# Optimization experiments

Hardware: AMD Instinct MI355X
Metric: run time of the kernel (lower is better)

Reference implementation:

```python
import jax, jax.numpy as jnp
import numpy as np

D_MODEL = 192; D_INNER = 384; N_STATE = 16; D_CONV = 4; DT_RANK = 12; DEPTH = 24
PATCH = 16; STRIDE = 16; IMG = 128; EPS = 1e-5


def _ln(x, w, b):
    m = jnp.mean(x, -1, keepdims=True)
    v = jnp.mean((x - m) ** 2, -1, keepdims=True)
    return (x - m) * jax.lax.rsqrt(v + EPS) * w + b


def _mamba_dir(xz, cw, cb, xpw, dpw, dpb, Alog, Dv):
    # xz: (B, L, 2*d_inner); one direction of the bidirectional Mamba mixer
    xp, z = jnp.split(xz, 2, axis=-1)               # (B,L,di) each
    xc = jnp.transpose(xp, (0, 2, 1))               # (B,di,L)
    xc = jnp.pad(xc, ((0, 0), (0, 0), (D_CONV - 1, 0)))  # causal pad
    xc = jax.lax.conv_general_dilated(
        xc, cw, (1,), 'VALID',
        dimension_numbers=('NCH', 'OIH', 'NCH'),
        feature_group_count=D_INNER) + cb[None, :, None]
    u = jax.nn.silu(jnp.transpose(xc, (0, 2, 1)))   # (B,L,di)
    dbl = u @ xpw.T                                  # (B,L,dt_rank+2N)
    dt, Bm, Cm = jnp.split(dbl, [DT_RANK, DT_RANK + N_STATE], axis=-1)
    dt = jax.nn.softplus(dt @ dpw.T + dpb)           # (B,L,di)
    A = -jnp.exp(Alog)                               # (di,N)
    dA = jnp.exp(dt[..., None] * A)                  # (B,L,di,N)
    dBu = (dt * u)[..., None] * Bm[:, :, None, :]    # (B,L,di,N)

    def comb(c1, c2):
        a1, b1 = c1
        a2, b2 = c2
        return a1 * a2, a2 * b1 + b2

    _, h = jax.lax.associative_scan(comb, (dA, dBu), axis=1)
    y = jnp.einsum('bldn,bln->bld', h, Cm) + u * Dv
    return y * jax.nn.silu(z)


def _forward(x, patch_w, patch_b, ln_w, ln_b, in_w,
             cf_w, cf_b, xpf_w, dtf_w, dtf_b, Alog_f, D_f,
             cbk_w, cbk_b, xpb_w, dtb_w, dtb_b, Alog_b, D_b,
             out_w, nf_w, nf_b, head_w, head_b):
    B = x.shape[0]
    p = jax.lax.conv_general_dilated(
        x, patch_w, (STRIDE,) * 3, 'VALID',
        dimension_numbers=('NCDHW', 'OIDHW', 'NCDHW')) + patch_b[None, :, None, None, None]
    hidden = p.reshape(B, D_MODEL, -1).transpose(0, 2, 1)  # (B, L=512, D)
    residual = jnp.zeros_like(hidden)

    xs = (ln_w, ln_b, in_w, cf_w, cf_b, xpf_w, dtf_w, dtf_b, Alog_f, D_f,
          cbk_w, cbk_b, xpb_w, dtb_w, dtb_b, Alog_b, D_b, out_w)

    def step(carry, pl):
        hidden, residual = carry
        (lw, lb, iw, cfw, cfb, xpf, dwf, dbf, Af, Dfv,
         cbw, cbb, xpb, dwb, dbb, Ab, Dbv, ow) = pl
        residual = residual + hidden
        hn = _ln(residual, lw, lb)
        xz = hn @ iw.T                               # (B,L,2di)
        yf = _mamba_dir(xz, cfw, cfb, xpf, dwf, dbf, Af, Dfv)
        yb = jnp.flip(_mamba_dir(jnp.flip(xz, 1), cbw, cbb, xpb, dwb, dbb, Ab, Dbv), 1)
        hidden = (yf + yb) @ ow.T
        return (hidden, residual), None

    (hidden, residual), _ = jax.lax.scan(step, (hidden, residual), xs)
    final = _ln(residual + hidden, nf_w, nf_b)
    feat = final[:, -1, :]                           # final_pool_type='none' -> last token
    return feat @ head_w.T + head_b


def setup_inputs() -> dict:
    key = jax.random.key(0)
    ks = jax.random.split(key, 16)
    rn = lambda k, s, sc=0.02: jax.random.normal(k, s, jnp.float32) * sc
    d = {}
    d['x'] = jax.random.normal(ks[0], (1, 1, IMG, IMG, IMG), jnp.float32)
    d['patch_w'] = rn(ks[1], (D_MODEL, 1, PATCH, PATCH, PATCH), 0.05)
    d['patch_b'] = jnp.zeros((D_MODEL,), jnp.float32)
    d['ln_w'] = jnp.ones((DEPTH, D_MODEL), jnp.float32)
    d['ln_b'] = jnp.zeros((DEPTH, D_MODEL), jnp.float32)
    d['in_w'] = rn(ks[2], (DEPTH, 2 * D_INNER, D_MODEL))
    d['cf_w'] = rn(ks[3], (DEPTH, D_INNER, 1, D_CONV), 0.2)
    d['cf_b'] = jnp.zeros((DEPTH, D_INNER), jnp.float32)
    d['xpf_w'] = rn(ks[4], (DEPTH, DT_RANK + 2 * N_STATE, D_INNER))
    d['dtf_w'] = rn(ks[5], (DEPTH, D_INNER, DT_RANK), 0.1)
    d['dtf_b'] = jnp.full((DEPTH, D_INNER), -4.6, jnp.float32)  # softplus -> dt~0.01
    d['Alog_f'] = jnp.log(jnp.broadcast_to(jnp.arange(1, N_STATE + 1, dtype=jnp.float32), (DEPTH, D_INNER, N_STATE)))
    d['D_f'] = jnp.ones((DEPTH, D_INNER), jnp.float32)
    d['cbk_w'] = rn(ks[6], (DEPTH, D_INNER, 1, D_CONV), 0.2)
    d['cbk_b'] = jnp.zeros((DEPTH, D_INNER), jnp.float32)
    d['xpb_w'] = rn(ks[7], (DEPTH, DT_RANK + 2 * N_STATE, D_INNER))
    d['dtb_w'] = rn(ks[8], (DEPTH, D_INNER, DT_RANK), 0.1)
    d['dtb_b'] = jnp.full((DEPTH, D_INNER), -4.6, jnp.float32)
    d['Alog_b'] = jnp.log(jnp.broadcast_to(jnp.arange(1, N_STATE + 1, dtype=jnp.float32), (DEPTH, D_INNER, N_STATE)))
    d['D_b'] = jnp.ones((DEPTH, D_INNER), jnp.float32)
    d['out_w'] = rn(ks[9], (DEPTH, D_MODEL, D_INNER))
    d['nf_w'] = jnp.ones((D_MODEL,), jnp.float32)
    d['nf_b'] = jnp.zeros((D_MODEL,), jnp.float32)
    d['head_w'] = rn(ks[10], (2, D_MODEL))
    d['head_b'] = jnp.zeros((2,), jnp.float32)
    return d


def reference(x, patch_w, patch_b, ln_w, ln_b, in_w,
              cf_w, cf_b, xpf_w, dtf_w, dtf_b, Alog_f, D_f,
              cbk_w, cbk_b, xpb_w, dtb_w, dtb_b, Alog_b, D_b,
              out_w, nf_w, nf_b, head_w, head_b):
    return _forward(x, patch_w, patch_b, ln_w, ln_b, in_w,
                    cf_w, cf_b, xpf_w, dtf_w, dtf_b, Alog_f, D_f,
                    cbk_w, cbk_b, xpb_w, dtb_w, dtb_b, Alog_b, D_b,
                    out_w, nf_w, nf_b, head_w, head_b)
```

## Files before the change

### kernel.cpp

```cpp
#include <hip/hip_runtime.h>
#include <hip/hip_bf16.h>

#define D_MODEL 192
#define D_INNER 384
#define N_STATE 16
#define DT_RANK 12
#define DEPTH 24
#define SEQ 512
#define NCHUNK 8
#define CLEN 64
#define TS 68
#define AS 33
#define PART_STRIDE (SEQ * D_MODEL)
#define USTR (SEQ * D_INNER)
#define KSPLIT 16
#define NBLK 512
#define FSTR 32

typedef __hip_bfloat16 bf16;
typedef unsigned short u16;
typedef unsigned long long u64;

__device__ __forceinline__ float silu_f(float x) { return x / (1.f + __expf(-x)); }
__device__ __forceinline__ float softplus_f(float x) {
    return (x > 20.f) ? x : log1pf(__expf(x));
}
__device__ __forceinline__ float bf2f(unsigned u) {
    return __uint_as_float(u << 16);
}
__device__ __forceinline__ u16 f2bu(float f) {
    bf16 b = __float2bfloat16(f);
    return *reinterpret_cast<u16*>(&b);
}

__device__ __forceinline__ float aload(const float* p) {
    return __hip_atomic_load(p, __ATOMIC_RELAXED, __HIP_MEMORY_SCOPE_AGENT);
}
__device__ __forceinline__ void astore(float* p, float v) {
    __hip_atomic_store(p, v, __ATOMIC_RELAXED, __HIP_MEMORY_SCOPE_AGENT);
}
__device__ __forceinline__ unsigned aloadu(const unsigned* p) {
    return __hip_atomic_load(p, __ATOMIC_RELAXED, __HIP_MEMORY_SCOPE_AGENT);
}
__device__ __forceinline__ void astoreu(unsigned* p, unsigned v) {
    __hip_atomic_store(p, v, __ATOMIC_RELAXED, __HIP_MEMORY_SCOPE_AGENT);
}
__device__ __forceinline__ float2 aload2(const float* p) {
    const u64 v = __hip_atomic_load((const u64*)p, __ATOMIC_RELAXED, __HIP_MEMORY_SCOPE_AGENT);
    return make_float2(__uint_as_float((unsigned)v), __uint_as_float((unsigned)(v >> 32)));
}
__device__ __forceinline__ void astore2(float* p, float x, float y) {
    const u64 v = (u64)__float_as_uint(x) | ((u64)__float_as_uint(y) << 32);
    __hip_atomic_store((u64*)p, v, __ATOMIC_RELAXED, __HIP_MEMORY_SCOPE_AGENT);
}
__device__ __forceinline__ float4 aload4v(const float* p) {
    const float2 a = aload2(p), b = aload2(p + 2);
    return make_float4(a.x, a.y, b.x, b.y);
}
__device__ __forceinline__ void astore4v(float* p, float4 v) {
    astore2(p, v.x, v.y); astore2(p + 2, v.z, v.w);
}

template<typename T> __device__ __forceinline__ float ld(const void* p, long i) {
    return ((const float*)p)[i];
}
template<> __device__ __forceinline__ float ld<bf16>(const void* p, long i) {
    return bf2f(((const u16*)p)[i]);
}
template<typename T> __device__ __forceinline__ float4 ld4(const void* p, long i) {
    return *(const float4*)((const float*)p + i);
}
template<> __device__ __forceinline__ float4 ld4<bf16>(const void* p, long i) {
    const ushort4 v = *(const ushort4*)((const u16*)p + i);
    return make_float4(bf2f(v.x), bf2f(v.y), bf2f(v.z), bf2f(v.w));
}
template<typename T> __device__ __forceinline__ void st(void* p, int i, float v) {
    ((float*)p)[i] = v;
}
template<> __device__ __forceinline__ void st<bf16>(void* p, int i, float v) {
    ((bf16*)p)[i] = __float2bfloat16(v);
}
__device__ __forceinline__ float dot4(const float4& a, const float4& b) {
    return a.x * b.x + a.y * b.y + a.z * b.z + a.w * b.w;
}
__device__ __forceinline__ void ld8b(const u16* p, float4& a, float4& b) {
    const uint4 u = *(const uint4*)p;
    a.x = bf2f(u.x & 0xffffu); a.y = bf2f(u.x >> 16);
    a.z = bf2f(u.y & 0xffffu); a.w = bf2f(u.y >> 16);
    b.x = bf2f(u.z & 0xffffu); b.y = bf2f(u.z >> 16);
    b.z = bf2f(u.w & 0xffffu); b.w = bf2f(u.w >> 16);
}
__device__ __forceinline__ float4 ld4b(const u16* p) {
    const uint2 u = *(const uint2*)p;
    return make_float4(bf2f(u.x & 0xffffu), bf2f(u.x >> 16),
                       bf2f(u.y & 0xffffu), bf2f(u.y >> 16));
}

__device__ __forceinline__ void post_flag(unsigned* fl, unsigned v, int tid) {
    asm volatile("s_waitcnt vmcnt(0)" ::: "memory");
    __syncthreads();
    if (tid == 0) astoreu(fl, v);
}
__device__ __forceinline__ void wait_flag(const unsigned* fl, unsigned v) {
    int spins = 0;
    while (aloadu(fl) < v) {
        if (++spins > (1 << 20)) break;
        __builtin_amdgcn_s_sleep(1);
    }
}

__device__ __forceinline__ void gbar(unsigned* bar, unsigned target, bool fence) {
    asm volatile("s_waitcnt vmcnt(0)" ::: "memory");
    __syncthreads();
    const int bid = blockIdx.x, tid = threadIdx.x;
    unsigned* gen0 = bar + 512 * FSTR;
    if (tid == 0) {
        if (fence) __threadfence();
        astoreu(&bar[bid * FSTR], target);
    }
    if (bid == 0) {
        int spins = 0;
        for (;;) {
            const unsigned va = aloadu(&bar[tid * FSTR]);
            const unsigned vb = aloadu(&bar[(tid + 256) * FSTR]);
            const bool ok = (va >= target) && (vb >= target);
            if (__syncthreads_and(ok)) break;
            if (++spins > (1 << 20)) break;
            __builtin_amdgcn_s_sleep(1);
        }
        if (tid == 0) astoreu(gen0, target);
    } else if (tid == 0) {
        int spins = 0;
        if (bid < 16) {
            while (aloadu(gen0) < target) {
                if (++spins > (1 << 20)) break;
                __builtin_amdgcn_s_sleep(2);
            }
            astoreu(&gen0[bid * FSTR], target);
        } else if (bid < 32) {
            while (aloadu(gen0) < target) {
                if (++spins > (1 << 20)) break;
                __builtin_amdgcn_s_sleep(2);
            }
        } else {
            unsigned* rl = &gen0[(bid >> 5) * FSTR];
            while (aloadu(rl) < target) {
                if (++spins > (1 << 20)) break;
                __builtin_amdgcn_s_sleep(2);
            }
        }
    }
    if (fence && tid == 0) __threadfence();
    __syncthreads();
}

__device__ void cvtB(const void* s, u16* d, long n, long g, long str, int isb) {
    if (isb) {
        const u16* p = (const u16*)s;
        for (long i = g * 4; i < n; i += str * 4) *(ushort4*)(d + i) = *(const ushort4*)(p + i);
    } else {
        const float* p = (const float*)s;
        for (long i = g * 4; i < n; i += str * 4) {
            const float4 v = *(const float4*)(p + i);
            ushort4 o; o.x = f2bu(v.x); o.y = f2bu(v.y); o.z = f2bu(v.z); o.w = f2bu(v.w);
            *(ushort4*)(d + i) = o;
        }
    }
}
__device__ void cvtF(const void* s, float* d, long n, long g, long str, int isb) {
    if (isb) {
        const u16* p = (const u16*)s;
        for (long i = g * 4; i < n; i += str * 4) {
            const ushort4 v = *(const ushort4*)(p + i);
            *(float4*)(d + i) = make_float4(bf2f(v.x), bf2f(v.y), bf2f(v.z), bf2f(v.w));
        }
    } else {
        const float* p = (const float*)s;
        for (long i = g * 4; i < n; i += str * 4) *(float4*)(d + i) = *(const float4*)(p + i);
    }
}
__device__ void cvtNA(const void* s, float* d, long n, long g, long str, int isb) {
    if (isb) {
        const u16* p = (const u16*)s;
        for (long i = g * 4; i < n; i += str * 4) {
            const ushort4 v = *(const ushort4*)(p + i);
            *(float4*)(d + i) = make_float4(-__expf(bf2f(v.x)), -__expf(bf2f(v.y)),
                                            -__expf(bf2f(v.z)), -__expf(bf2f(v.w)));
        }
    } else {
        const float* p = (const float*)s;
        for (long i = g * 4; i < n; i += str * 4) {
            const float4 v = *(const float4*)(p + i);
            *(float4*)(d + i) = make_float4(-__expf(v.x), -__expf(v.y), -__expf(v.z), -__expf(v.w));
        }
    }
}

template<typename T>
__device__ void final_phase(int tid, const float* res, const float* y, const void* ow,
                            const void* nw, const void* nb, const void* hw, const void* hb,
                            void* out, float* syf, float* f, float* red) {
    for (int i = tid; i < D_INNER; i += 256)
        syf[i] = aload(&y[(long)511 * D_INNER + i]) + aload(&y[(long)USTR + 511 * D_INNER + i]);
    __syncthreads();
    float v = 0.f;
    if (tid < D_MODEL) {
        float acc = 0.f;
        const long wrow = (long)(DEPTH - 1) * D_MODEL * D_INNER + (long)tid * D_INNER;
        for (int k = 0; k < D_INNER; k += 4)
            acc += dot4(ld4<T>(ow, wrow + k), *(const float4*)&syf[k]);
        v = aload(&res[511 * D_MODEL + tid]) + acc;
    }
    float s = v;
    #pragma unroll
    for (int o = 32; o > 0; o >>= 1) s += __shfl_down(s, o, 64);
    if ((tid & 63) == 0 && tid < D_MODEL) red[tid >> 6] = s;
    __syncthreads();
    const float mean = (red[0] + red[1] + red[2]) * (1.f / D_MODEL);
    const float d = (tid < D_MODEL) ? (v - mean) : 0.f;
    float s2 = d * d;
    #pragma unroll
    for (int o = 32; o > 0; o >>= 1) s2 += __shfl_down(s2, o, 64);
    if ((tid & 63) == 0 && tid < D_MODEL) red[3 + (tid >> 6)] = s2;
    __syncthreads();
    const float var = (red[3] + red[4] + red[5]) * (1.f / D_MODEL);
    if (tid < D_MODEL)
        f[tid] = d * rsqrtf(var + 1e-5f) * ld<T>(nw, tid) + ld<T>(nb, tid);
    __syncthreads();
    if (tid < 2) {
        float a2 = ld<T>(hb, tid);
        for (int c = 0; c < D_MODEL; ++c) a2 += f[c] * ld<T>(hw, tid * D_MODEL + c);
        st<T>(out, tid, a2);
    }
}

struct MegaArgs {
    const void *x, *pw, *pb, *lnw, *lnb, *inw, *cfw, *cfb, *xpfw, *dtfw, *dtfb, *Af, *Dfv;
    const void *cbw, *cbb, *xpbw, *dtbw, *dtbb, *Ab, *Dbv, *ow, *nfw, *nfb, *hw, *hb;
    void* out;
    unsigned* bar;
    float *hidC, *res0, *res1, *xz, *u, *dbl, *dt, *y, *chunkH, *chunkP;
    float *lnwF, *lnbF, *cbfF, *cbbF, *dtbfF, *dtbbF, *negAfF, *negAbF, *DfF, *DbF, *pbF;
    u16 *inwB, *owB, *xB, *pwB, *xpwfB, *xpwbB, *dtwfB, *dtwbB, *cwfB, *cwbB;
};

__global__ void init_kernel(unsigned* bar) {
    const int i = blockIdx.x * 256 + threadIdx.x;
    ((uint4*)bar)[i] = make_uint4(0, 0, 0, 0);
}

__global__ void __launch_bounds__(256, 2) mega_kernel(MegaArgs a) {
    __shared__ float smem[6144];
    const int bid = blockIdx.x;
    const int tid = threadIdx.x;
    unsigned* bar = a.bar;
    unsigned* scanR = a.bar + 528 * FSTR;
    unsigned* aflag = a.bar + 912 * FSTR;
    unsigned* bflag = a.bar + 1168 * FSTR;
    unsigned gen_ctr = 0;
    const int isb = (((const unsigned*)a.lnw)[0] != 0x3F800000u);

    {
        const long g = (long)bid * 256 + tid;
        const long str = (long)NBLK * 256;
        cvtB(a.inw,  a.inwB,  3538944, g, str, isb);
        cvtB(a.ow,   a.owB,   1769472, g, str, isb);
        cvtB(a.x,    a.xB,    2097152, g, str, isb);
        cvtB(a.pw,   a.pwB,    786432, g, str, isb);
        cvtB(a.xpfw, a.xpwfB,  405504, g, str, isb);
        cvtB(a.xpbw, a.xpwbB,  405504, g, str, isb);
        cvtB(a.dtfw, a.dtwfB,  110592, g, str, isb);
        cvtB(a.dtbw, a.dtwbB,  110592, g, str, isb);
        cvtB(a.cfw,  a.cwfB,    36864, g, str, isb);
        cvtB(a.cbw,  a.cwbB,    36864, g, str, isb);
        cvtF(a.lnw,  a.lnwF,     4608, g, str, isb);
        cvtF(a.lnb,  a.lnbF,     4608, g, str, isb);
        cvtF(a.cfb,  a.cbfF,     9216, g, str, isb);
        cvtF(a.cbb,  a.cbbF,     9216, g, str, isb);
        cvtF(a.dtfb, a.dtbfF,    9216, g, str, isb);
        cvtF(a.dtbb, a.dtbbF,    9216, g, str, isb);
        cvtF(a.pb,   a.pbF,       192, g, str, isb);
        cvtNA(a.Af,  a.negAfF,  147456, g, str, isb);
        cvtNA(a.Ab,  a.negAbF,  147456, g, str, isb);
        cvtF(a.Dfv,  a.DfF,      9216, g, str, isb);
        cvtF(a.Dbv,  a.DbF,      9216, g, str, isb);
    }
    gbar(bar, ++gen_ctr, true);

    {
        float* As_ = smem;
        float* Ws  = smem + 1056;
        const int ty = tid >> 4, tx = tid & 15;
        for (int unit = bid; unit < 768; unit += NBLK) {
            const int mt = unit & 15, nt = (unit >> 4) % 3, ks = unit / 48;
            const int m0 = mt * 32, n0 = nt * 64, kk0 = ks * 256;
            float acc[2][4] = {};
            for (int kk = kk0; kk < kk0 + 256; kk += 32) {
                for (int e = tid; e < 1024; e += 256) {
                    const int m = e >> 5, k = e & 31;
                    const int kid = kk + k, t = m0 + m;
                    const int dz = kid >> 8, dy = (kid >> 4) & 15, dx = kid & 15;
                    const int pz = t >> 6, py = (t >> 3) & 7, px = t & 7;
                    As_[k * AS + m] = bf2f(a.xB[(long)(pz * 16 + dz) * 16384 + (py * 16 + dy) * 128 + (px * 16 + dx)]);
                }
                for (int e = tid; e < 2048; e += 256) {
                    const int n = e >> 5, k = e & 31;
                    Ws[k * TS + n] = bf2f(a.pwB[(long)(n0 + n) * 4096 + kk + k]);
                }
                __syncthreads();
                #pragma unroll 8
                for (int k = 0; k < 32; ++k) {
                    const float a0 = As_[k * AS + ty * 2];
                    const float a1 = As_[k * AS + ty * 2 + 1];
                    const float4 w4 = *(const float4*)&Ws[k * TS + tx * 4];
                    acc[0][0] += a0 * w4.x; acc[0][1] += a0 * w4.y;
                    acc[0][2] += a0 * w4.z; acc[0][3] += a0 * w4.w;
                    acc[1][0] += a1 * w4.x; acc[1][1] += a1 * w4.y;
                    acc[1][2] += a1 * w4.z; acc[1][3] += a1 * w4.w;
                }
                __syncthreads();
            }
            float* C = a.hidC + (long)ks * PART_STRIDE;
            #pragma unroll
            for (int i = 0; i < 2; ++i) {
                float4 o4 = make_float4(acc[i][0], acc[i][1], acc[i][2], acc[i][3]);
                if (ks == 0) {
                    o4.x += a.pbF[n0 + tx * 4 + 0];
                    o4.y += a.pbF[n0 + tx * 4 + 1];
                    o4.z += a.pbF[n0 + tx * 4 + 2];
                    o4.w += a.pbF[n0 + tx * 4 + 3];
                }
                astore4v(&C[(m0 + ty * 2 + i) * D_MODEL + n0 + tx * 4], o4);
            }
        }
    }
    gbar(bar, ++gen_ctr, false);

    const int ch = tid >> 4, np = tid & 15;
    float* sU  = smem;
    float* sDT = smem + 1024;
    float* sBC = smem + 2048;
    float* sZ  = smem + 4096;
    float* sY  = smem + 5120;

    for (int l = 0; l < DEPTH; ++l) {
        const int first = (l == 0);
        const unsigned lv = (unsigned)(l + 1);
        const float* resIn = (l & 1) ? a.res1 : a.res0;
        float* resOut      = (l & 1) ? a.res0 : a.res1;

        if (bid < 256) {
            float* sy  = smem;
            float* lnS = smem + 768;
            float* hnS = smem + 1152;
            const int t0 = bid * 2;
            if (!first) {
                for (int j = tid; j < 384; j += 256) {
                    const int tt = j / 192, d2 = (j - tt * 192) * 2;
                    const long o = (long)(t0 + tt) * D_INNER + d2;
                    const float2 v1 = aload2(&a.y[o]);
                    const float2 v2 = aload2(&a.y[(long)USTR + o]);
                    sy[tt * D_INNER + d2]     = v1.x + v2.x;
                    sy[tt * D_INNER + d2 + 1] = v1.y + v2.y;
                }
            }
            __syncthreads();
            if (tid < D_MODEL) {
                float accB[2];
                if (first) {
                    #pragma unroll
                    for (int tt = 0; tt < 2; ++tt) {
                        float s = 0.f;
                        #pragma unroll
                        for (int sp = 0; sp < KSPLIT; ++sp)
                            s += aload(&a.hidC[(long)sp * PART_STRIDE + (t0 + tt) * D_MODEL + tid]);
                        accB[tt] = s;
                    }
                } else {
                    accB[0] = accB[1] = 0.f;
                    const u16* wr = a.owB + (long)(l - 1) * D_MODEL * D_INNER + (long)tid * D_INNER;
                    for (int k = 0; k < D_INNER; k += 8) {
                        float4 va, vb;
                        ld8b(wr + k, va, vb);
                        accB[0] += dot4(va, *(const float4*)&sy[k]) + dot4(vb, *(const float4*)&sy[k + 4]);
                        accB[1] += dot4(va, *(const float4*)&sy[D_INNER + k]) + dot4(vb, *(const float4*)&sy[D_INNER + k + 4]);
                    }
                }
                #pragma unroll
                for (int tt = 0; tt < 2; ++tt) {
                    const float rv = accB[tt] + (first ? 0.f : aload(&resIn[(t0 + tt) * D_MODEL + tid]));
                    lnS[tt * D_MODEL + tid] = rv;
                    astore(&resOut[(t0 + tt) * D_MODEL + tid], rv);
                }
            }
            __syncthreads();
            {
                const int w = tid >> 6, lane = tid & 63;
                if (w < 2) {
                    const float v0 = lnS[w * D_MODEL + lane];
                    const float v1 = lnS[w * D_MODEL + lane + 64];
                    const float v2 = lnS[w * D_MODEL + lane + 128];
                    float s = v0 + v1 + v2;
                    #pragma unroll
                    for (int o = 32; o > 0; o >>= 1) s += __shfl_xor(s, o, 64);
                    const float mean = s * (1.f / D_MODEL);
                    const float d0 = v0 - mean, d1 = v1 - mean, d2 = v2 - mean;
                    float s2 = d0 * d0 + d1 * d1 + d2 * d2;
                    #pragma unroll
                    for (int o = 32; o > 0; o >>= 1) s2 += __shfl_xor(s2, o, 64);
                    const float rstd = rsqrtf(s2 * (1.f / D_MODEL) + 1e-5f);
                    hnS[w * D_MODEL + lane]       = d0 * rstd * a.lnwF[l * D_MODEL + lane]       + a.lnbF[l * D_MODEL + lane];
                    hnS[w * D_MODEL + lane + 64]  = d1 * rstd * a.lnwF[l * D_MODEL + lane + 64]  + a.lnbF[l * D_MODEL + lane + 64];
                    hnS[w * D_MODEL + lane + 128] = d2 * rstd * a.lnwF[l * D_MODEL + lane + 128] + a.lnbF[l * D_MODEL + lane + 128];
                }
            }
            __syncthreads();
            float accD[3][2] = {};
            const u16* w0 = a.inwB + (long)l * 2 * D_INNER * D_MODEL;
            for (int k = 0; k < D_MODEL; k += 8) {
                #pragma unroll
                for (int r = 0; r < 3; ++r) {
                    float4 va, vb;
                    ld8b(w0 + (long)(tid + r * 256) * D_MODEL + k, va, vb);
                    #pragma unroll
                    for (int tt = 0; tt < 2; ++tt) {
                        accD[r][tt] += dot4(va, *(const float4*)&hnS[tt * D_MODEL + k])
                                     + dot4(vb, *(const float4*)&hnS[tt * D_MODEL + k + 4]);
                    }
                }
            }
            #pragma unroll
            for (int r = 0; r < 3; ++r)
                #pragma unroll
                for (int tt = 0; tt < 2; ++tt)
                    astore(&a.xz[(long)(t0 + tt) * 2 * D_INNER + tid + r * 256], accD[r][tt]);
            post_flag(&aflag[bid * FSTR], lv, tid);
        }

        {
            const int dir = bid >> 8, bb = bid & 255;
            int lo, hi;
            if (dir == 0) { lo = bb >= 2 ? bb - 2 : 0; hi = bb; }
            else { lo = bb <= 255 ? (255 - bb > 0 ? 255 - bb : 0) : 0;
                   hi = 257 - bb <= 255 ? 257 - bb : 255; }
            if (tid <= hi - lo) wait_flag(&aflag[(lo + tid) * FSTR], lv);
            __syncthreads();

            float* su   = smem;
            float* dblP = smem + 768;
            float* dblS = smem + 960;
            const u16* cwB   = dir ? a.cwbB  : a.cwfB;
            const float* cbF = dir ? a.cbbF  : a.cbfF;
            const u16* xpwB  = dir ? a.xpwbB : a.xpwfB;
            const u16* dtwB  = dir ? a.dtwbB : a.dtwfB;
            const float* dtbF = dir ? a.dtbbF : a.dtbfF;
            const int t0 = bb * 2;
            float* ub = a.u + (long)dir * USTR;
            for (int j = tid; j < 384; j += 256) {
                const int tt = j / 192, d2 = (j - tt * 192) * 2;
                const int t = t0 + tt;
                float4 wa, wb;
                ld8b(cwB + (long)(l * D_INNER + d2) * 4, wa, wb);
                const float cw0[4] = {wa.x, wa.y, wa.z, wa.w};
                const float cw1[4] = {wb.x, wb.y, wb.z, wb.w};
                float acc0 = cbF[l * D_INNER + d2];
                float acc1 = cbF[l * D_INNER + d2 + 1];
                #pragma unroll
                for (int k = 0; k < 4; ++k) {
                    const int ii = t + k - 3;
                    if (ii >= 0) {
                        const int src = dir ? (511 - ii) : ii;
                        const float2 xv = aload2(&a.xz[(long)src * 2 * D_INNER + d2]);
                        acc0 += xv.x * cw0[k];
                        acc1 += xv.y * cw1[k];
                    }
                }
                const float u0 = silu_f(acc0), u1 = silu_f(acc1);
                su[tt * D_INNER + d2] = u0;
                su[tt * D_INNER + d2 + 1] = u1;
                astore2(&ub[(long)t * D_INNER + d2], u0, u1);
            }
            __syncthreads();
            if (tid < 176) {
                const int half = tid / 88;
                const int r = tid - half * 88;
                const int tt = r / 44, out = r - tt * 44;
                const u16* wr = xpwB + (long)(l * 44 + out) * D_INNER;
                const int k0 = half * 192;
                float acc = 0.f;
                for (int k = k0; k < k0 + 192; k += 8) {
                    float4 va, vb;
                    ld8b(wr + k, va, vb);
                    acc += dot4(va, *(const float4*)&su[tt * D_INNER + k])
                         + dot4(vb, *(const float4*)&su[tt * D_INNER + k + 4]);
                }
                dblP[half * 96 + tt * 48 + out] = acc;
            }
            __syncthreads();
            if (tid < 88) {
                const int tt = tid / 44, out = tid - tt * 44;
                const float s = dblP[tt * 48 + out] + dblP[96 + tt * 48 + out];
                dblS[tt * 48 + out] = s;
                astore(&a.dbl[(long)dir * SEQ * 44 + (long)(t0 + tt) * 44 + out], s);
            }
            __syncthreads();
            float* dtp = a.dt + (long)dir * USTR;
            for (int j = tid; j < 384; j += 256) {
                const int tt = j / 192, d2 = (j - tt * 192) * 2;
                const u16* wr = dtwB + (long)(l * D_INNER + d2) * DT_RANK;
                float4 A0, B0; ld8b(wr, A0, B0);
                const float4 C0 = ld4b(wr + 8);
                float4 A1, B1; ld8b(wr + 12, A1, B1);
                const float4 C1 = ld4b(wr + 20);
                const float* ds = &dblS[tt * 48];
                const float4 ds0 = *(const float4*)ds;
                const float4 ds1 = *(const float4*)(ds + 4);
                const float4 ds2 = *(const float4*)(ds + 8);
                const float acc0 = dtbF[l * D_INNER + d2]
                    + dot4(A0, ds0) + dot4(B0, ds1) + dot4(C0, ds2);
                const float acc1 = dtbF[l * D_INNER + d2 + 1]
                    + dot4(A1, ds0) + dot4(B1, ds1) + dot4(C1, ds2);
                astore2(&dtp[(long)(t0 + tt) * D_INNER + d2],
                        softplus_f(acc0), softplus_f(acc1));
            }
            post_flag(&bflag[bid * FSTR], lv, tid);
        }

        if (bid < 384) {
            const int dg = bid % 24, chunk = (bid / 24) & 7, dir2 = bid / 192;
            if (tid < 32) wait_flag(&bflag[(dir2 * 256 + chunk * 32 + tid) * FSTR], lv);
            __syncthreads();
            const int d0 = dg * 16, d = d0 + ch;
            const int t0s = chunk * CLEN;
            const float* ub  = a.u  + (long)dir2 * USTR;
            const float* dtp = a.dt + (long)dir2 * USTR;
            const float* db  = a.dbl + (long)dir2 * SEQ * 44;
            {
                const int t = tid >> 2, dl4 = (tid & 3) * 4;
                const int tg = t0s + t;
                const long base = (long)tg * D_INNER + d0 + dl4;
                *(float4*)&sU[t * 16 + dl4]  = aload4v(&ub[base]);
                *(float4*)&sDT[t * 16 + dl4] = aload4v(&dtp[base]);
                const int out_l = dir2 ? (511 - tg) : tg;
                *(float4*)&sZ[t * 16 + dl4] = aload4v(&a.xz[(long)out_l * 2 * D_INNER + D_INNER + d0 + dl4]);
            }
            for (int i = tid; i < 512; i += 256) {
                const int t = i >> 3, j4 = (i & 7) * 4;
                *(float4*)&sBC[t * 32 + j4] = aload4v(&db[(long)(t0s + t) * 44 + DT_RANK + j4]);
            }
            const float* negA = dir2 ? a.negAbF : a.negAfF;
            const float Areg = negA[(long)(l * D_INNER + d) * N_STATE + np];
            const float Dval = (dir2 ? a.DbF : a.DfF)[l * D_INNER + d];
            __syncthreads();
            float h = 0.f, dts = 0.f;
            for (int t = 0; t < CLEN; ++t) {
                const float dtv = sDT[t * 16 + ch];
                h = __expf(dtv * Areg) * h + (dtv * sU[t * 16 + ch]) * sBC[t * 32 + np];
                dts += dtv;
            }
            const long cb = ((long)(dir2 * NCHUNK + chunk) * D_INNER + d) * N_STATE + np;
            astore(&a.chunkH[cb], h);
            astore(&a.chunkP[cb], __expf(Areg * dts));
            post_flag(&scanR[((dir2 * NCHUNK + chunk) * 24 + dg) * FSTR], lv, tid);
            if (tid < chunk) wait_flag(&scanR[((dir2 * NCHUNK + tid) * 24 + dg) * FSTR], lv);
            __syncthreads();
            float hs[NCHUNK - 1], ps[NCHUNK - 1];
            #pragma unroll
            for (int c = 0; c < NCHUNK - 1; ++c) {
                if (c < chunk) {
                    const long cbb = ((long)(dir2 * NCHUNK + c) * D_INNER + d) * N_STATE + np;
                    hs[c] = aload(&a.chunkH[cbb]);
                    ps[c] = aload(&a.chunkP[cbb]);
                }
            }
            float h0 = 0.f;
            #pragma unroll
            for (int c = 0; c < NCHUNK - 1; ++c)
                if (c < chunk) h0 = ps[c] * h0 + hs[c];
            h = h0;
            for (int t = 0; t < CLEN; ++t) {
                const float dtv = sDT[t * 16 + ch];
                const float uv = sU[t * 16 + ch];
                h = __expf(dtv * Areg) * h + (dtv * uv) * sBC[t * 32 + np];
                float part = h * sBC[t * 32 + 16 + np];
                part += __shfl_xor(part, 1, 64);
                part += __shfl_xor(part, 2, 64);
                part += __shfl_xor(part, 4, 64);
                part += __shfl_xor(part, 8, 64);
                if (np == 0)
                    sY[t * 16 + ch] = (part + uv * Dval) * silu_f(sZ[t * 16 + ch]);
            }
            __syncthreads();
            {
                const int t = tid >> 2, dl4 = (tid & 3) * 4;
                const int tg = t0s + t;
                const int out_l = dir2 ? (511 - tg) : tg;
                float* yb = a.y + (long)dir2 * USTR;
                astore4v(&yb[(long)out_l * D_INNER + d0 + dl4], *(float4*)&sY[t * 16 + dl4]);
            }
        }
        gbar(bar, ++gen_ctr, false);
    }

    if (bid == 0) {
        float* syf = smem;
        float* f   = smem + 384;
        float* red = smem + 576;
        if (isb) final_phase<bf16>(tid, a.res0, a.y, a.ow, a.nfw, a.nfb, a.hw, a.hb, a.out, syf, f, red);
        else     final_phase<float>(tid, a.res0, a.y, a.ow, a.nfw, a.nfb, a.hw, a.hb, a.out, syf, f, red);
    }
}

extern "C" void kernel_launch(void* const* d_in, const int* in_sizes, int n_in,
                              void* d_out, int out_size, void* d_ws, size_t ws_size,
                              hipStream_t stream) {
    (void)in_sizes; (void)n_in; (void)out_size; (void)ws_size;
    const void* x    = d_in[0];
    const void* pw   = d_in[1];
    const void* pb   = d_in[2];
    const void* lnw  = d_in[3];
    const void* lnb  = d_in[4];
    const void* inw  = d_in[5];
    const void* cfw  = d_in[6];
    const void* cfb  = d_in[7];
    const void* xpfw = d_in[8];
    const void* dtfw = d_in[9];
    const void* dtfb = d_in[10];
    const void* Af   = d_in[11];
    const void* Dfv  = d_in[12];
    const void* cbw  = d_in[13];
    const void* cbb  = d_in[14];
    const void* xpbw = d_in[15];
    const void* dtbw = d_in[16];
    const void* dtbb = d_in[17];
    const void* Ab   = d_in[18];
    const void* Dbv  = d_in[19];
    const void* ow   = d_in[20];
    const void* nfw  = d_in[21];
    const void* nfb  = d_in[22];
    const void* hw   = d_in[23];
    const void* hb   = d_in[24];

    unsigned* bar = (unsigned*)d_ws;
    float* w = (float*)((char*)d_ws + 262144);
    float* hidC   = w;  w += KSPLIT * PART_STRIDE;
    float* res0   = w;  w += PART_STRIDE;
    float* res1   = w;  w += PART_STRIDE;
    float* xz     = w;  w += SEQ * 2 * D_INNER;
    float* u      = w;  w += 2 * USTR;
    float* dbl    = w;  w += 2 * SEQ * 44;
    float* dt     = w;  w += 2 * USTR;
    float* y      = w;  w += 2 * USTR;
    float* chunkH = w;  w += 2 * NCHUNK * D_INNER * N_STATE;
    float* chunkP = w;  w += 2 * NCHUNK * D_INNER * N_STATE;
    float* lnwF = w;  w += 4608;
    float* lnbF = w;  w += 4608;
    float* cbfF = w;  w += 9216;
    float* cbbF = w;  w += 9216;
    float* dtbfF = w; w += 9216;
    float* dtbbF = w; w += 9216;
    float* negAfF = w; w += 147456;
    float* negAbF = w; w += 147456;
    float* DfF = w;   w += 9216;
    float* DbF = w;   w += 9216;
    float* pbF = w;   w += 192;
    u16* b = (u16*)w;
    u16* inwB  = b;  b += 3538944;
    u16* owB   = b;  b += 1769472;
    u16* xB    = b;  b += 2097152;
    u16* pwB   = b;  b += 786432;
    u16* xpwfB = b;  b += 405504;
    u16* xpwbB = b;  b += 405504;
    u16* dtwfB = b;  b += 110592;
    u16* dtwbB = b;  b += 110592;
    u16* cwfB  = b;  b += 36864;
    u16* cwbB  = b;  b += 36864;

    MegaArgs ma;
    ma.x = x; ma.pw = pw; ma.pb = pb; ma.lnw = lnw; ma.lnb = lnb; ma.inw = inw;
    ma.cfw = cfw; ma.cfb = cfb; ma.xpfw = xpfw; ma.dtfw = dtfw; ma.dtfb = dtfb;
    ma.Af = Af; ma.Dfv = Dfv; ma.cbw = cbw; ma.cbb = cbb; ma.xpbw = xpbw;
    ma.dtbw = dtbw; ma.dtbb = dtbb; ma.Ab = Ab; ma.Dbv = Dbv; ma.ow = ow;
    ma.nfw = nfw; ma.nfb = nfb; ma.hw = hw; ma.hb = hb; ma.out = d_out;
    ma.bar = bar;
    ma.hidC = hidC; ma.res0 = res0; ma.res1 = res1; ma.xz = xz; ma.u = u;
    ma.dbl = dbl; ma.dt = dt; ma.y = y; ma.chunkH = chunkH; ma.chunkP = chunkP;
    ma.lnwF = lnwF; ma.lnbF = lnbF; ma.cbfF = cbfF; ma.cbbF = cbbF;
    ma.dtbfF = dtbfF; ma.dtbbF = dtbbF; ma.negAfF = negAfF; ma.negAbF = negAbF;
    ma.DfF = DfF; ma.DbF = DbF; ma.pbF = pbF;
    ma.inwB = inwB; ma.owB = owB; ma.xB = xB; ma.pwB = pwB;
    ma.xpwfB = xpwfB; ma.xpwbB = xpwbB; ma.dtwfB = dtwfB; ma.dtwbB = dtwbB;
    ma.cwfB = cwfB; ma.cwbB = cwbB;

    init_kernel<<<64, 256, 0, stream>>>(bar);
    mega_kernel<<<NBLK, 256, 0, stream>>>(ma);
}
```

Baseline: 1.955 ms.

## Replace every other per-layer grid barrier with fine-grained y flags and double buffers

Per-chunk y-ready flags are added so that the next layer's LN/in-proj blocks wait only for the scan chunks they consume, instead of a global grid barrier after every layer. The barrier now runs only on odd layers. Intermediate buffers (xz, u, dt, dbl, chunk states) are double-buffered by layer parity so adjacent layers cannot overwrite each other's data. This costs extra workspace and flag traffic, and risks races if the parity and flag dependencies are incomplete.

```diff
diff --git a/kernel.cpp b/kernel.cpp
--- a/kernel.cpp
+++ b/kernel.cpp
@@ -16,6 +16,8 @@
 #define KSPLIT 16
 #define NBLK 512
 #define FSTR 32
+#define XZSTR (SEQ * 2 * D_INNER)
+#define CHSTR (2 * NCHUNK * D_INNER * N_STATE)
 
 typedef __hip_bfloat16 bf16;
 typedef unsigned short u16;
@@ -257,6 +259,7 @@
     unsigned* scanR = a.bar + 528 * FSTR;
     unsigned* aflag = a.bar + 912 * FSTR;
     unsigned* bflag = a.bar + 1168 * FSTR;
+    unsigned* yflag = a.bar + 1680 * FSTR;
     unsigned gen_ctr = 0;
     const int isb = (((const unsigned*)a.lnw)[0] != 0x3F800000u);
 
@@ -346,10 +349,27 @@
     for (int l = 0; l < DEPTH; ++l) {
         const int first = (l == 0);
         const unsigned lv = (unsigned)(l + 1);
-        const float* resIn = (l & 1) ? a.res1 : a.res0;
-        float* resOut      = (l & 1) ? a.res0 : a.res1;
+        const int par = l & 1;
+        float* xzP = a.xz + (long)par * XZSTR;
+        float* uP  = a.u  + (long)par * (2 * USTR);
+        float* dtP = a.dt + (long)par * (2 * USTR);
+        float* dbG = a.dbl + (long)par * (2 * SEQ * 44);
+        float* chH = a.chunkH + (long)par * CHSTR;
+        float* chPb = a.chunkP + (long)par * CHSTR;
+        const float* resIn = par ? a.res1 : a.res0;
+        float* resOut      = par ? a.res0 : a.res1;
 
         if (bid < 256) {
+            if (par) {
+                if (tid < 48) {
+                    const int dd = tid / 24, dg = tid - dd * 24;
+                    const int cf = bid >> 5;
+                    const int cb = (511 - 2 * bid) >> 6;
+                    const int cc = dd ? cb : cf;
+                    wait_flag(&yflag[((dd * NCHUNK + cc) * 24 + dg) * FSTR], (unsigned)l);
+                }
+                __syncthreads();
+            }
             float* sy  = smem;
             float* lnS = smem + 768;
             float* hnS = smem + 1152;
@@ -433,7 +453,7 @@
             for (int r = 0; r < 3; ++r)
                 #pragma unroll
                 for (int tt = 0; tt < 2; ++tt)
-                    astore(&a.xz[(long)(t0 + tt) * 2 * D_INNER + tid + r * 256], accD[r][tt]);
+                    astore(&xzP[(long)(t0 + tt) * 2 * D_INNER + tid + r * 256], accD[r][tt]);
             post_flag(&aflag[bid * FSTR], lv, tid);
         }
 
@@ -455,7 +475,7 @@
             const u16* dtwB  = dir ? a.dtwbB : a.dtwfB;
             const float* dtbF = dir ? a.dtbbF : a.dtbfF;
             const int t0 = bb * 2;
-            float* ub = a.u + (long)dir * USTR;
+            float* ub = uP + (long)dir * USTR;
             for (int j = tid; j < 384; j += 256) {
                 const int tt = j / 192, d2 = (j - tt * 192) * 2;
                 const int t = t0 + tt;
@@ -470,7 +490,7 @@
                     const int ii = t + k - 3;
                     if (ii >= 0) {
                         const int src = dir ? (511 - ii) : ii;
-                        const float2 xv = aload2(&a.xz[(long)src * 2 * D_INNER + d2]);
+                        const float2 xv = aload2(&xzP[(long)src * 2 * D_INNER + d2]);
                         acc0 += xv.x * cw0[k];
                         acc1 += xv.y * cw1[k];
                     }
@@ -501,10 +521,10 @@
                 const int tt = tid / 44, out = tid - tt * 44;
                 const float s = dblP[tt * 48 + out] + dblP[96 + tt * 48 + out];
                 dblS[tt * 48 + out] = s;
-                astore(&a.dbl[(long)dir * SEQ * 44 + (long)(t0 + tt) * 44 + out], s);
-            }
-            __syncthreads();
-            float* dtp = a.dt + (long)dir * USTR;
+                astore(&dbG[(long)dir * SEQ * 44 + (long)(t0 + tt) * 44 + out], s);
+            }
+            __syncthreads();
+            float* dtp = dtP + (long)dir * USTR;
             for (int j = tid; j < 384; j += 256) {
                 const int tt = j / 192, d2 = (j - tt * 192) * 2;
                 const u16* wr = dtwB + (long)(l * D_INNER + d2) * DT_RANK;
@@ -532,9 +552,9 @@
             __syncthreads();
             const int d0 = dg * 16, d = d0 + ch;
             const int t0s = chunk * CLEN;
-            const float* ub  = a.u  + (long)dir2 * USTR;
-            const float* dtp = a.dt + (long)dir2 * USTR;
-            const float* db  = a.dbl + (long)dir2 * SEQ * 44;
+            const float* ub  = uP  + (long)dir2 * USTR;
+            const float* dtp = dtP + (long)dir2 * USTR;
+            const float* db  = dbG + (long)dir2 * SEQ * 44;
             {
                 const int t = tid >> 2, dl4 = (tid & 3) * 4;
                 const int tg = t0s + t;
@@ -542,7 +562,7 @@
                 *(float4*)&sU[t * 16 + dl4]  = aload4v(&ub[base]);
                 *(float4*)&sDT[t * 16 + dl4] = aload4v(&dtp[base]);
                 const int out_l = dir2 ? (511 - tg) : tg;
-                *(float4*)&sZ[t * 16 + dl4] = aload4v(&a.xz[(long)out_l * 2 * D_INNER + D_INNER + d0 + dl4]);
+                *(float4*)&sZ[t * 16 + dl4] = aload4v(&xzP[(long)out_l * 2 * D_INNER + D_INNER + d0 + dl4]);
             }
             for (int i = tid; i < 512; i += 256) {
                 const int t = i >> 3, j4 = (i & 7) * 4;
@@ -558,9 +578,9 @@
                 h = __expf(dtv * Areg) * h + (dtv * sU[t * 16 + ch]) * sBC[t * 32 + np];
                 dts += dtv;
             }
-            const long cb = ((long)(dir2 * NCHUNK + chunk) * D_INNER + d) * N_STATE + np;
-            astore(&a.chunkH[cb], h);
-            astore(&a.chunkP[cb], __expf(Areg * dts));
+            const long cb2 = ((long)(dir2 * NCHUNK + chunk) * D_INNER + d) * N_STATE + np;
+            astore(&chH[cb2], h);
+            astore(&chPb[cb2], __expf(Areg * dts));
             post_flag(&scanR[((dir2 * NCHUNK + chunk) * 24 + dg) * FSTR], lv, tid);
             if (tid < chunk) wait_flag(&scanR[((dir2 * NCHUNK + tid) * 24 + dg) * FSTR], lv);
             __syncthreads();
@@ -569,8 +589,8 @@
             for (int c = 0; c < NCHUNK - 1; ++c) {
                 if (c < chunk) {
                     const long cbb = ((long)(dir2 * NCHUNK + c) * D_INNER + d) * N_STATE + np;
-                    hs[c] = aload(&a.chunkH[cbb]);
-                    ps[c] = aload(&a.chunkP[cbb]);
+                    hs[c] = aload(&chH[cbb]);
+                    ps[c] = aload(&chPb[cbb]);
                 }
             }
             float h0 = 0.f;
@@ -598,8 +618,9 @@
                 float* yb = a.y + (long)dir2 * USTR;
                 astore4v(&yb[(long)out_l * D_INNER + d0 + dl4], *(float4*)&sY[t * 16 + dl4]);
             }
-        }
-        gbar(bar, ++gen_ctr, false);
+            post_flag(&yflag[((dir2 * NCHUNK + chunk) * 24 + dg) * FSTR], lv, tid);
+        }
+        if (par) gbar(bar, ++gen_ctr, false);
     }
 
     if (bid == 0) {
@@ -642,17 +663,17 @@
     const void* hb   = d_in[24];
 
     unsigned* bar = (unsigned*)d_ws;
-    float* w = (float*)((char*)d_ws + 262144);
+    float* w = (float*)((char*)d_ws + 327680);
     float* hidC   = w;  w += KSPLIT * PART_STRIDE;
     float* res0   = w;  w += PART_STRIDE;
     float* res1   = w;  w += PART_STRIDE;
-    float* xz     = w;  w += SEQ * 2 * D_INNER;
-    float* u      = w;  w += 2 * USTR;
-    float* dbl    = w;  w += 2 * SEQ * 44;
-    float* dt     = w;  w += 2 * USTR;
+    float* xz     = w;  w += 2 * XZSTR;
+    float* u      = w;  w += 2 * 2 * USTR;
+    float* dbl    = w;  w += 2 * 2 * SEQ * 44;
+    float* dt     = w;  w += 2 * 2 * USTR;
     float* y      = w;  w += 2 * USTR;
-    float* chunkH = w;  w += 2 * NCHUNK * D_INNER * N_STATE;
-    float* chunkP = w;  w += 2 * NCHUNK * D_INNER * N_STATE;
+    float* chunkH = w;  w += 2 * CHSTR;
+    float* chunkP = w;  w += 2 * CHSTR;
     float* lnwF = w;  w += 4608;
     float* lnbF = w;  w += 4608;
     float* cbfF = w;  w += 9216;
@@ -692,6 +713,6 @@
     ma.xpwfB = xpwfB; ma.xpwbB = xpwbB; ma.dtwfB = dtwfB; ma.dtwbB = dtwbB;
     ma.cwfB = cwfB; ma.cwbB = cwbB;
 
-    init_kernel<<<64, 256, 0, stream>>>(bar);
+    init_kernel<<<80, 256, 0, stream>>>(bar);
     mega_kernel<<<NBLK, 256, 0, stream>>>(ma);
 }
```

After: 1.934 ms. About the same (-1.1%).
